# Kernel tuning notes

Hardware: AMD Instinct MI355X
Metric: run time of the kernel (lower is better)

The kernel has to match this reference:

```python
import jax, jax.numpy as jnp
import numpy as np

TEMPERATURE = 0.1
NORMALIZE = True


def setup_inputs() -> dict:
    key = jax.random.key(0)
    k1, k2 = jax.random.split(key)
    B, D = 4096, 512
    return {
        "z_i": jax.random.normal(k1, (B, D), dtype=jnp.float32),
        "z_j": jax.random.normal(k2, (B, D), dtype=jnp.float32),
    }


def _l2norm(x):
    return x / jnp.sqrt(jnp.sum(x * x, axis=-1, keepdims=True))


def reference(z_i, z_j):
    if NORMALIZE:
        z_i = _l2norm(z_i)
        z_j = _l2norm(z_j)
    B = z_i.shape[0]

    inv_t = 1.0 / TEMPERATURE
    logits_aa = (z_i @ z_i.T) * inv_t  # [B, B]
    logits_bb = (z_j @ z_j.T) * inv_t
    logits_ab = (z_i @ z_j.T) * inv_t
    logits_ba = (z_j @ z_i.T) * inv_t

    # Static off-diagonal column indices: row i keeps cols 0..B-1 except i,
    # in ascending order (matches torch boolean-mask row-major extraction).
    j = jnp.arange(B - 1)[None, :]
    i = jnp.arange(B)[:, None]
    idx = j + (j >= i)  # [B, B-1] int32

    take = lambda m: jnp.take_along_axis(m, idx, axis=1)  # [B, B-1]

    pos = jnp.concatenate([jnp.diagonal(logits_ab), jnp.diagonal(logits_ba)])[:, None]  # [2B, 1]
    neg_a = jnp.concatenate([take(logits_aa), take(logits_ab)], axis=1)  # [B, 2(B-1)]
    neg_b = jnp.concatenate([take(logits_ba), take(logits_bb)], axis=1)
    neg = jnp.concatenate([neg_a, neg_b], axis=0)  # [2B, 2(B-1)]

    logits = jnp.concatenate([pos, neg], axis=1)  # [2B, 2B-1]
    logp = jax.nn.log_softmax(logits, axis=1)
    # Original forward uses labels = torch.ones(2B).long() -> target class 1.
    loss = -jnp.mean(logp[:, 1])
    return loss
```

## Files before the change

### kernel.cpp

```cpp
#include <hip/hip_runtime.h>
#include <hip/hip_bf16.h>
#include <hip/hip_fp8.h>


#define BB 4096
#define DD 512
#define NN 8192
#define TILE 128
#define NBLK 2080

typedef __attribute__((ext_vector_type(4)))  float f32x4;
typedef __attribute__((ext_vector_type(16))) float f32x16;
typedef __attribute__((ext_vector_type(4)))  int   i32x4;
typedef __attribute__((ext_vector_type(8)))  int   i32x8;

#define AS1 __attribute__((address_space(1)))
#define AS3 __attribute__((address_space(3)))
static __device__ __forceinline__ void gload_lds16(const void* g, void* l) {
    __builtin_amdgcn_global_load_lds((const AS1 void*)g, (AS3 void*)l, 16, 0, 0);
}

__global__ __launch_bounds__(256)
void normalize_kernel(const float* __restrict__ zi, const float* __restrict__ zj,
                      unsigned char* __restrict__ M, float* __restrict__ rowsum) {
    const int wave = threadIdx.x >> 6;
    const int lane = threadIdx.x & 63;
    const int row  = blockIdx.x * 4 + wave;
    if (threadIdx.x < 4) rowsum[blockIdx.x * 4 + threadIdx.x] = 0.f;
    const float* src = (row < BB) ? (zi + (size_t)row * DD)
                                  : (zj + (size_t)(row - BB) * DD);
    float4 v0 = ((const float4*)src)[lane * 2 + 0];
    float4 v1 = ((const float4*)src)[lane * 2 + 1];
    float ss = v0.x*v0.x + v0.y*v0.y + v0.z*v0.z + v0.w*v0.w
             + v1.x*v1.x + v1.y*v1.y + v1.z*v1.z + v1.w*v1.w;
    #pragma unroll
    for (int off = 1; off <= 32; off <<= 1) ss += __shfl_xor(ss, off);
    const float inv = rsqrtf(ss);
    const float vals[8] = {v0.x*inv, v0.y*inv, v0.z*inv, v0.w*inv,
                           v1.x*inv, v1.y*inv, v1.z*inv, v1.w*inv};
    union { long u; unsigned char b[8]; } pk;
    #pragma unroll
    for (int j = 0; j < 8; ++j)
        pk.b[j] = __hip_cvt_float_to_fp8(vals[j], __HIP_SATFINITE, __HIP_E4M3);
    ((long*)(M + (size_t)row * DD))[lane] = pk.u;
}

__global__ __launch_bounds__(256, 2)
void gram_lse_kernel(const unsigned char* __restrict__ Mg,
                     float* __restrict__ rowsum, float* __restrict__ targets) {
    __shared__ __align__(16) char Bs[TILE * DD];

    const int d = blockIdx.x;
    const int p = (d & 7) * 260 + (d >> 3);
    int by = (int)((sqrtf(8.0f * (float)p + 1.0f) - 1.0f) * 0.5f);
    while ((by + 1) * (by + 2) / 2 <= p) ++by;
    while (by * (by + 1) / 2 > p) --by;
    const int bx = p - by * (by + 1) / 2;

    const int rowBase = bx * TILE;
    const int colBase = by * TILE;
    const bool diag = (bx == by);
    const int tid  = threadIdx.x;
    const int wave = tid >> 6;
    const int lane = tid & 63;
    const int l31 = lane & 31;
    const int h0  = lane >> 5;

    #pragma unroll
    for (int i = 0; i < 16; ++i) {
        const int row = i * 8 + (tid >> 5);
        const int sg  = (tid & 31) ^ (row & 31);
        gload_lds16(Mg + (size_t)(colBase + row) * DD + sg * 16,
                    Bs + ((size_t)i * 256 + tid) * 16);
    }

    const unsigned char* Arow = Mg + (size_t)(rowBase + wave * 32 + l31) * DD + h0 * 32;
    i32x4 a4[16];
    #pragma unroll
    for (int t2 = 0; t2 < 16; ++t2)
        a4[t2] = *(const i32x4*)(Arow + (t2 >> 1) * 64 + (t2 & 1) * 16);

    __syncthreads();

    f32x16 acc[4] = {};
    const int rb0 = l31 * DD;
    #pragma unroll
    for (int t = 0; t < 8; ++t) {
        const int g0 = t * 4 + h0 * 2;
        const int p0 = (g0 ^ l31) * 16;
        const int p1 = ((g0 ^ 1) ^ l31) * 16;
        const i32x8 a = __builtin_shufflevector(a4[2 * t], a4[2 * t + 1],
                                                0, 1, 2, 3, 4, 5, 6, 7);
        #pragma unroll
        for (int ni = 0; ni < 4; ++ni) {
            const char* rbase = Bs + rb0 + ni * 32 * DD;
            i32x4 lo = *(const i32x4*)(rbase + p0);
            i32x4 hi = *(const i32x4*)(rbase + p1);
            i32x8 b = __builtin_shufflevector(lo, hi, 0, 1, 2, 3, 4, 5, 6, 7);
            acc[ni] = __builtin_amdgcn_mfma_scale_f32_32x32x64_f8f6f4(
                a, b, acc[ni], 0, 0, 0, 0x7F7F7F7F, 0, 0x7F7F7F7F);
        }
    }

    const float C10 = 14.42695040888963f;
    float rs[16] = {};
    float cs[4]  = {};
    #pragma unroll
    for (int ni = 0; ni < 4; ++ni) {
        const int gcol = colBase + ni * 32 + l31;
        #pragma unroll
        for (int r = 0; r < 16; ++r) {
            const int lrow = (r & 3) + 8 * (r >> 2) + 4 * h0;
            const int grow = rowBase + wave * 32 + lrow;
            float e = __builtin_amdgcn_exp2f(fmaf(acc[ni][r], C10, -C10));
            if (grow == gcol) e = 0.f;
            rs[r] += e;
            cs[ni] += e;
            if (rowBase == 0 && grow < 2) {
                const int j0 = ((gcol & (BB - 1)) == 0) ? 1 : 0;
                if (grow == j0) targets[gcol] = 10.f * acc[ni][r];
            }
        }
    }
    #pragma unroll
    for (int m = 1; m <= 16; m <<= 1)
        #pragma unroll
        for (int r = 0; r < 16; ++r)
            rs[r] += __shfl_xor(rs[r], m);
    if (l31 == 0) {
        #pragma unroll
        for (int r = 0; r < 16; ++r)
            atomicAdd(&rowsum[rowBase + wave * 32
                              + (r & 3) + 8 * (r >> 2) + 4 * h0], rs[r]);
    }
    if (!diag) {
        #pragma unroll
        for (int ni = 0; ni < 4; ++ni)
            cs[ni] += __shfl_xor(cs[ni], 32);
        if (h0 == 0) {
            #pragma unroll
            for (int ni = 0; ni < 4; ++ni)
                atomicAdd(&rowsum[colBase + ni * 32 + l31], cs[ni]);
        }
    }
}

__global__ __launch_bounds__(1024)
void finalize_kernel(const float* __restrict__ rowsum,
                     const float* __restrict__ targets, float* __restrict__ out) {
    const int tid = threadIdx.x;
    float s = 0.f;
    #pragma unroll
    for (int t = tid; t < NN; t += 1024)
        s += targets[t] - 10.f - __logf(rowsum[t]);
    #pragma unroll
    for (int off = 1; off <= 32; off <<= 1) s += __shfl_xor(s, off);
    __shared__ float red[16];
    if ((tid & 63) == 0) red[tid >> 6] = s;
    __syncthreads();
    if (tid == 0) {
        float t = 0.f;
        #pragma unroll
        for (int i = 0; i < 16; ++i) t += red[i];
        out[0] = -t / (float)NN;
    }
}

extern "C" void kernel_launch(void* const* d_in, const int* in_sizes, int n_in,
                              void* d_out, int out_size, void* d_ws, size_t ws_size,
                              hipStream_t stream) {
    const float* zi = (const float*)d_in[0];
    const float* zj = (const float*)d_in[1];

    unsigned char* M = (unsigned char*)d_ws;
    float* rowsum  = (float*)((char*)d_ws + (size_t)NN * DD);
    float* targets = rowsum + NN;
    float* out = (float*)d_out;

    normalize_kernel<<<NN / 4, 256, 0, stream>>>(zi, zj, M, rowsum);
    gram_lse_kernel<<<NBLK, 256, 0, stream>>>(M, rowsum, targets);
    finalize_kernel<<<1, 1024, 0, stream>>>(rowsum, targets, out);
}
```

Baseline: 108.8 us.

## Replace rowsum atomics with per-panel partial buffers and parallel reduction

The Gram tile kernel now writes its row and column exp-sums into a per-panel partial array instead of doing global atomicAdds. Column sums are combined across waves in LDS first. A new multi-block reduce kernel sums the 64 partials per row, takes the log and atomically accumulates the loss, and a tiny kernel writes the final scalar. The A-operand fragments are also streamed with a two-step register prefetch instead of all being loaded up front, which lowers register pressure. The cost is an extra kernel launch and a 2 MB partial buffer that must be written and read back.

```diff
diff --git a/kernel.cpp b/kernel.cpp
--- a/kernel.cpp
+++ b/kernel.cpp
@@ -7,6 +7,7 @@
 #define DD 512
 #define NN 8192
 #define TILE 128
+#define NPAN 64
 #define NBLK 2080
 
 typedef __attribute__((ext_vector_type(4)))  float f32x4;
@@ -22,11 +23,11 @@
 
 __global__ __launch_bounds__(256)
 void normalize_kernel(const float* __restrict__ zi, const float* __restrict__ zj,
-                      unsigned char* __restrict__ M, float* __restrict__ rowsum) {
+                      unsigned char* __restrict__ M, float* __restrict__ wacc) {
     const int wave = threadIdx.x >> 6;
     const int lane = threadIdx.x & 63;
     const int row  = blockIdx.x * 4 + wave;
-    if (threadIdx.x < 4) rowsum[blockIdx.x * 4 + threadIdx.x] = 0.f;
+    if (blockIdx.x == 0 && threadIdx.x == 0) wacc[0] = 0.f;
     const float* src = (row < BB) ? (zi + (size_t)row * DD)
                                   : (zj + (size_t)(row - BB) * DD);
     float4 v0 = ((const float4*)src)[lane * 2 + 0];
@@ -47,7 +48,7 @@
 
 __global__ __launch_bounds__(256, 2)
 void gram_lse_kernel(const unsigned char* __restrict__ Mg,
-                     float* __restrict__ rowsum, float* __restrict__ targets) {
+                     float* __restrict__ rpart, float* __restrict__ targets) {
     __shared__ __align__(16) char Bs[TILE * DD];
 
     const int d = blockIdx.x;
@@ -74,23 +75,26 @@
                     Bs + ((size_t)i * 256 + tid) * 16);
     }
 
-    const unsigned char* Arow = Mg + (size_t)(rowBase + wave * 32 + l31) * DD + h0 * 32;
-    i32x4 a4[16];
-    #pragma unroll
-    for (int t2 = 0; t2 < 16; ++t2)
-        a4[t2] = *(const i32x4*)(Arow + (t2 >> 1) * 64 + (t2 & 1) * 16);
+    const unsigned char* Arow =
+        Mg + (size_t)(rowBase + wave * 32 + l31) * DD + h0 * 32;
 
     __syncthreads();
 
     f32x16 acc[4] = {};
     const int rb0 = l31 * DD;
+    i32x4 c0a = *(const i32x4*)(Arow +   0), c0b = *(const i32x4*)(Arow +  16);
+    i32x4 c1a = *(const i32x4*)(Arow +  64), c1b = *(const i32x4*)(Arow +  80);
     #pragma unroll
     for (int t = 0; t < 8; ++t) {
+        const i32x8 a = __builtin_shufflevector(c0a, c0b, 0, 1, 2, 3, 4, 5, 6, 7);
+        c0a = c1a; c0b = c1b;
+        if (t + 2 < 8) {
+            c1a = *(const i32x4*)(Arow + (t + 2) * 64);
+            c1b = *(const i32x4*)(Arow + (t + 2) * 64 + 16);
+        }
         const int g0 = t * 4 + h0 * 2;
         const int p0 = (g0 ^ l31) * 16;
         const int p1 = ((g0 ^ 1) ^ l31) * 16;
-        const i32x8 a = __builtin_shufflevector(a4[2 * t], a4[2 * t + 1],
-                                                0, 1, 2, 3, 4, 5, 6, 7);
         #pragma unroll
         for (int ni = 0; ni < 4; ++ni) {
             const char* rbase = Bs + rb0 + ni * 32 * DD;
@@ -130,40 +134,50 @@
     if (l31 == 0) {
         #pragma unroll
         for (int r = 0; r < 16; ++r)
-            atomicAdd(&rowsum[rowBase + wave * 32
-                              + (r & 3) + 8 * (r >> 2) + 4 * h0], rs[r]);
+            rpart[(size_t)by * NN + rowBase + wave * 32
+                  + (r & 3) + 8 * (r >> 2) + 4 * h0] = rs[r];
     }
     if (!diag) {
         #pragma unroll
         for (int ni = 0; ni < 4; ++ni)
             cs[ni] += __shfl_xor(cs[ni], 32);
+        float* cpart = (float*)Bs;
+        __syncthreads();
         if (h0 == 0) {
             #pragma unroll
             for (int ni = 0; ni < 4; ++ni)
-                atomicAdd(&rowsum[colBase + ni * 32 + l31], cs[ni]);
+                cpart[wave * TILE + ni * 32 + l31] = cs[ni];
+        }
+        __syncthreads();
+        if (tid < TILE) {
+            float v = cpart[tid] + cpart[TILE + tid]
+                    + cpart[2 * TILE + tid] + cpart[3 * TILE + tid];
+            rpart[(size_t)bx * NN + colBase + tid] = v;
         }
     }
 }
 
-__global__ __launch_bounds__(1024)
-void finalize_kernel(const float* __restrict__ rowsum,
-                     const float* __restrict__ targets, float* __restrict__ out) {
-    const int tid = threadIdx.x;
+__global__ __launch_bounds__(256)
+void reduce_kernel(const float* __restrict__ rpart,
+                   const float* __restrict__ targets, float* __restrict__ wacc) {
+    const int i = blockIdx.x * 256 + threadIdx.x;
     float s = 0.f;
+    #pragma unroll 8
+    for (int sl = 0; sl < NPAN; ++sl)
+        s += rpart[(size_t)sl * NN + i];
+    float term = targets[i] - 10.f - __logf(s);
     #pragma unroll
-    for (int t = tid; t < NN; t += 1024)
-        s += targets[t] - 10.f - __logf(rowsum[t]);
-    #pragma unroll
-    for (int off = 1; off <= 32; off <<= 1) s += __shfl_xor(s, off);
-    __shared__ float red[16];
-    if ((tid & 63) == 0) red[tid >> 6] = s;
+    for (int off = 1; off <= 32; off <<= 1) term += __shfl_xor(term, off);
+    __shared__ float red[4];
+    if ((threadIdx.x & 63) == 0) red[threadIdx.x >> 6] = term;
     __syncthreads();
-    if (tid == 0) {
-        float t = 0.f;
-        #pragma unroll
-        for (int i = 0; i < 16; ++i) t += red[i];
-        out[0] = -t / (float)NN;
-    }
+    if (threadIdx.x == 0)
+        atomicAdd(wacc, red[0] + red[1] + red[2] + red[3]);
+}
+
+__global__ void write_kernel(const float* __restrict__ wacc,
+                             float* __restrict__ out) {
+    out[0] = -wacc[0] / (float)NN;
 }
 
 extern "C" void kernel_launch(void* const* d_in, const int* in_sizes, int n_in,
@@ -173,11 +187,13 @@
     const float* zj = (const float*)d_in[1];
 
     unsigned char* M = (unsigned char*)d_ws;
-    float* rowsum  = (float*)((char*)d_ws + (size_t)NN * DD);
-    float* targets = rowsum + NN;
+    float* rpart   = (float*)((char*)d_ws + (size_t)NN * DD);
+    float* targets = rpart + (size_t)NPAN * NN;
+    float* wacc    = targets + NN;
     float* out = (float*)d_out;
 
-    normalize_kernel<<<NN / 4, 256, 0, stream>>>(zi, zj, M, rowsum);
-    gram_lse_kernel<<<NBLK, 256, 0, stream>>>(M, rowsum, targets);
-    finalize_kernel<<<1, 1024, 0, stream>>>(rowsum, targets, out);
+    normalize_kernel<<<NN / 4, 256, 0, stream>>>(zi, zj, M, wacc);
+    gram_lse_kernel<<<NBLK, 256, 0, stream>>>(M, rpart, targets);
+    reduce_kernel<<<NN / 256, 256, 0, stream>>>(rpart, targets, wacc);
+    write_kernel<<<1, 1, 0, stream>>>(wacc, out);
 }
```

New measurement: 107.2 us. Within noise of the previous version (-1.5%).
